# Kernel tuning notes

Hardware: AMD Instinct MI355X
Metric: run time of the kernel (lower is better)

The kernel has to match this reference:

```python
import jax, jax.numpy as jnp
import numpy as np

N_NODES = 170000
N_EDGES = 1200000
IN_DIM = 64
OUT_DIM = 40


def setup_inputs() -> dict:
    key = jax.random.key(0)
    k1, k2, k3, k4 = jax.random.split(key, 4)
    feats = jax.random.normal(k1, (N_NODES, IN_DIM), dtype=jnp.float32)
    # Linear layer params (Kaiming-ish scale)
    W = jax.random.normal(k2, (OUT_DIM, IN_DIM), dtype=jnp.float32) * (1.0 / np.sqrt(IN_DIM))
    b = jnp.zeros((OUT_DIM,), dtype=jnp.float32)
    src = jax.random.randint(k3, (N_EDGES,), 0, N_NODES, dtype=jnp.int64)
    dst = jax.random.randint(k4, (N_EDGES,), 0, N_NODES, dtype=jnp.int64)
    return {"feats": feats, "W": W, "b": b, "src": src, "dst": dst}


def reference(feats, W, b, src, dst):
    # DGL SGConv, k=1: symmetric normalization by in-degree^-1/2 on both sides.
    n = feats.shape[0]
    deg = jax.ops.segment_sum(jnp.ones_like(dst, dtype=feats.dtype), dst, num_segments=n)
    norm = jax.lax.rsqrt(jnp.maximum(deg, 1.0))  # clamp(min=1)
    h = feats * norm[:, None]                    # [N, D] pre-scale
    msgs = jnp.take(h, src, axis=0)              # [E, D] gather
    agg = jax.ops.segment_sum(msgs, dst, num_segments=n)  # [N, D] scatter-sum
    h = agg * norm[:, None]                      # post-scale
    out = jnp.einsum('nd,cd->nc', h, W) + b      # Linear(IN_DIM -> OUT_DIM)
    return out
```

## Files before the change

kernel.cpp:

```cpp
#include <hip/hip_runtime.h>
#include <hip/hip_bf16.h>

#define N_NODES 170000
#define N_EDGES 1200000
#define IN_DIM 64
#define OUT_DIM 40
#define PAD 32
#define ZW 20
#define MTILES (N_NODES / 16)
#define TFB ((MTILES + 3) / 4)
#define SEGS 8
#define SEG_SZ (N_NODES / SEGS)
#define SLICES 512
#define SLICE_E ((N_EDGES + SLICES - 1) / SLICES)
#define FILLB (SLICES * SEGS)
#define FUSED_BLOCKS (FILLB + TFB)
#define WS_DS32_OFF 36056576ULL
#define WS_SS32_OFF (WS_DS32_OFF + (size_t)N_EDGES * 4)
#define WS_NEED     (WS_SS32_OFF + (size_t)N_EDGES * 4)

typedef __attribute__((ext_vector_type(8))) short short8;
typedef __attribute__((ext_vector_type(4))) float f32x4;

__device__ __forceinline__ float bf2f(unsigned int u) {
    union { unsigned int i; float f; } v;
    v.i = u << 16;
    return v.f;
}

__device__ __forceinline__ unsigned short f2bf_bits(float x) {
    __hip_bfloat16 h = __float2bfloat16(x);
    union { __hip_bfloat16 h; unsigned short u; } c; c.h = h;
    return c.u;
}

__device__ __forceinline__ int load_idx(const void* p, int e, int is_i32) {
    return is_i32 ? ((const int*)p)[e] : (int)((const long long*)p)[e];
}

__global__ void __launch_bounds__(256) k_init(
    const unsigned short* __restrict__ Wraw, const unsigned short* __restrict__ braw,
    const unsigned int* __restrict__ dstraw, const unsigned int* __restrict__ srcraw,
    int* __restrict__ flags, unsigned short* __restrict__ Wb, float* __restrict__ bfv,
    int* __restrict__ cnt, int* __restrict__ ds32, int* __restrict__ ss32) {
    int tid = blockIdx.x * 256 + threadIdx.x;
    int gsz = (int)gridDim.x * 256;
    int4* c4 = (int4*)cnt;
    for (int i = tid; i < 42500; i += gsz) c4[i] = make_int4(0, 0, 0, 0);

    __shared__ int s_i32l;
    if (threadIdx.x == 0) s_i32l = 0;
    __syncthreads();
    if (dstraw[2 * threadIdx.x + 1] != 0u) atomicOr(&s_i32l, 1);
    __syncthreads();
    int is_i32 = s_i32l;

    if (!is_i32 && ds32) {
        const long long* d64 = (const long long*)dstraw;
        const long long* s64 = (const long long*)srcraw;
        for (int i = tid; i < N_EDGES; i += gsz) ds32[i] = (int)d64[i];
        for (int i = tid; i < N_EDGES; i += gsz) ss32[i] = (int)s64[i];
    }
    if (blockIdx.x != 0) return;

    __shared__ int s_f32;
    if (threadIdx.x == 0) s_f32 = 0;
    __syncthreads();
    for (int i = threadIdx.x; i < OUT_DIM * IN_DIM; i += 256) {
        float v = bf2f(Wraw[i]);
        if (!(fabsf(v) <= 100.0f)) atomicOr(&s_f32, 1);
    }
    __syncthreads();
    int is_f32 = s_f32;
    if (threadIdx.x == 0) { flags[0] = s_f32; flags[1] = is_i32; }
    for (int i = threadIdx.x; i < OUT_DIM * IN_DIM; i += 256)
        Wb[i] = is_f32 ? f2bf_bits(((const float*)Wraw)[i]) : Wraw[i];
    for (int i = threadIdx.x; i < OUT_DIM; i += 256)
        bfv[i] = is_f32 ? ((const float*)braw)[i] : bf2f(braw[i]);
}

__global__ void __launch_bounds__(256) k_fused(
    const void* __restrict__ src, const void* __restrict__ dst,
    int* __restrict__ cnt, int* __restrict__ slots,
    const void* __restrict__ feats, const unsigned short* __restrict__ Wb,
    unsigned short* __restrict__ Zp16, const int* __restrict__ flags,
    const int* __restrict__ ds32, const int* __restrict__ ss32) {
    int bid = blockIdx.x;
    int do_fill, id;
    if (bid < 2 * TFB) { do_fill = bid & 1; id = bid >> 1; }
    else               { do_fill = 1;       id = bid - TFB; }

    if (do_fill) {
        int is_i32 = flags[1];
        int seg   = id & 7;
        int slice = id >> 3;
        int lo = seg * SEG_SZ, hi = lo + SEG_SZ;
        int e0 = slice * SLICE_E;
        int e1 = e0 + SLICE_E; if (e1 > N_EDGES) e1 = N_EDGES;
        const int* dp = is_i32 ? (const int*)dst : ds32;
        const int* sp = is_i32 ? (const int*)src : ss32;
        if (dp) {
            int nE = e1 - e0;
            int nV = nE >> 2;
            const int4* dv = (const int4*)(dp + e0);
            const int4* sv = (const int4*)(sp + e0);
            for (int q = (int)threadIdx.x; q < nV; q += 256) {
                int4 d4 = dv[q];
                int4 s4 = sv[q];
                if (d4.x >= lo && d4.x < hi) {
                    int pos = atomicAdd(&cnt[d4.x], 1);
                    if (pos < PAD) slots[(size_t)d4.x * PAD + pos] = s4.x;
                }
                if (d4.y >= lo && d4.y < hi) {
                    int pos = atomicAdd(&cnt[d4.y], 1);
                    if (pos < PAD) slots[(size_t)d4.y * PAD + pos] = s4.y;
                }
                if (d4.z >= lo && d4.z < hi) {
                    int pos = atomicAdd(&cnt[d4.z], 1);
                    if (pos < PAD) slots[(size_t)d4.z * PAD + pos] = s4.z;
                }
                if (d4.w >= lo && d4.w < hi) {
                    int pos = atomicAdd(&cnt[d4.w], 1);
                    if (pos < PAD) slots[(size_t)d4.w * PAD + pos] = s4.w;
                }
            }
            int rem = nE & 3;
            if ((int)threadIdx.x < rem) {
                int e = e0 + (nV << 2) + (int)threadIdx.x;
                int d = dp[e];
                if (d >= lo && d < hi) {
                    int pos = atomicAdd(&cnt[d], 1);
                    if (pos < PAD) slots[(size_t)d * PAD + pos] = sp[e];
                }
            }
        } else {
            for (int e = e0 + (int)threadIdx.x; e < e1; e += 256) {
                int d = load_idx(dst, e, 0);
                if (d >= lo && d < hi) {
                    int s = load_idx(src, e, 0);
                    int pos = atomicAdd(&cnt[d], 1);
                    if (pos < PAD) slots[(size_t)d * PAD + pos] = s;
                }
            }
        }
    } else {
        int is_f32 = flags[0];
        int wave = id * 4 + (int)(threadIdx.x >> 6);
        int lane = threadIdx.x & 63;
        if (wave >= MTILES) return;
        int m = lane & 15;
        int quad = lane >> 4;
        int node0 = wave * 16;

        short8 a0, a1;
        if (is_f32) {
            const float* frow = (const float*)feats + (size_t)(node0 + m) * IN_DIM + quad * 8;
            float4 p0 = *(const float4*)(frow + 0);
            float4 p1 = *(const float4*)(frow + 4);
            float4 p2 = *(const float4*)(frow + 32);
            float4 p3 = *(const float4*)(frow + 36);
            a0[0] = (short)f2bf_bits(p0.x); a0[1] = (short)f2bf_bits(p0.y);
            a0[2] = (short)f2bf_bits(p0.z); a0[3] = (short)f2bf_bits(p0.w);
            a0[4] = (short)f2bf_bits(p1.x); a0[5] = (short)f2bf_bits(p1.y);
            a0[6] = (short)f2bf_bits(p1.z); a0[7] = (short)f2bf_bits(p1.w);
            a1[0] = (short)f2bf_bits(p2.x); a1[1] = (short)f2bf_bits(p2.y);
            a1[2] = (short)f2bf_bits(p2.z); a1[3] = (short)f2bf_bits(p2.w);
            a1[4] = (short)f2bf_bits(p3.x); a1[5] = (short)f2bf_bits(p3.y);
            a1[6] = (short)f2bf_bits(p3.z); a1[7] = (short)f2bf_bits(p3.w);
        } else {
            const unsigned short* frow = (const unsigned short*)feats + (size_t)(node0 + m) * IN_DIM + quad * 8;
            a0 = *(const short8*)(frow);
            a1 = *(const short8*)(frow + 32);
        }

        f32x4 c0 = {0.f, 0.f, 0.f, 0.f}, c1 = c0, c2 = c0;
#pragma unroll
        for (int t = 0; t < 3; t++) {
            int n = t * 16 + m;
            bool ok = (n < OUT_DIM);
            short8 b0, b1;
#pragma unroll
            for (int j = 0; j < 8; j++) { b0[j] = 0; b1[j] = 0; }
            if (ok) {
                const unsigned short* wrow = Wb + (size_t)n * IN_DIM + quad * 8;
                b0 = *(const short8*)(wrow);
                b1 = *(const short8*)(wrow + 32);
            }
            if (t == 0) {
                c0 = __builtin_amdgcn_mfma_f32_16x16x32_bf16(a0, b0, c0, 0, 0, 0);
                c0 = __builtin_amdgcn_mfma_f32_16x16x32_bf16(a1, b1, c0, 0, 0, 0);
            } else if (t == 1) {
                c1 = __builtin_amdgcn_mfma_f32_16x16x32_bf16(a0, b0, c1, 0, 0, 0);
                c1 = __builtin_amdgcn_mfma_f32_16x16x32_bf16(a1, b1, c1, 0, 0, 0);
            } else {
                c2 = __builtin_amdgcn_mfma_f32_16x16x32_bf16(a0, b0, c2, 0, 0, 0);
                c2 = __builtin_amdgcn_mfma_f32_16x16x32_bf16(a1, b1, c2, 0, 0, 0);
            }
        }

        int r0 = quad * 4;
#pragma unroll
        for (int r = 0; r < 4; r++) {
            size_t base = (size_t)(node0 + r0 + r) * OUT_DIM;
            Zp16[base + m]      = f2bf_bits(c0[r]);
            Zp16[base + 16 + m] = f2bf_bits(c1[r]);
            if (m < 8)
                Zp16[base + 32 + m] = f2bf_bits(c2[r]);
        }
    }
}

__global__ void __launch_bounds__(256) k_gather(
    const int* __restrict__ cnt, const int* __restrict__ slots,
    const unsigned int* __restrict__ Zp, const float* __restrict__ bfv,
    float* __restrict__ out) {
    int wid = (blockIdx.x * blockDim.x + threadIdx.x) >> 6;
    int lane = threadIdx.x & 63;
    if (wid >= N_NODES) return;
    int deg = cnt[wid];
    int dc = deg > PAD ? PAD : deg;
    const int* sl = slots + (size_t)wid * PAD;
    int myslot = sl[lane & 31];

    int grp = lane / 10;
    int cidx = lane - grp * 10;
    bool lact = (grp < 6);

    float a0 = 0.f, a1 = 0.f, a2 = 0.f, a3 = 0.f;
    if (dc > 0) {
        int rounds = (dc + 5) / 6;
        bool v = lact && (grp < dc);
        int s = __shfl(myslot, (v ? grp : 0) & 31);
        uint2 r = *(const uint2*)(Zp + (size_t)s * ZW + 2 * cidx);
        int cdeg = cnt[s];
        for (int rd = 1; rd < rounds; rd++) {
            int e1 = rd * 6 + grp;
            bool v1 = lact && (e1 < dc);
            int s1 = __shfl(myslot, (v1 ? e1 : 0) & 31);
            uint2 rn = *(const uint2*)(Zp + (size_t)s1 * ZW + 2 * cidx);
            int cn = cnt[s1];
            if (v) {
                float nvs = rsqrtf(cdeg > 1 ? (float)cdeg : 1.0f);
                a0 = fmaf(bf2f(r.x & 0xFFFFu), nvs, a0);
                a1 = fmaf(bf2f(r.x >> 16),     nvs, a1);
                a2 = fmaf(bf2f(r.y & 0xFFFFu), nvs, a2);
                a3 = fmaf(bf2f(r.y >> 16),     nvs, a3);
            }
            v = v1; r = rn; cdeg = cn;
        }
        if (v) {
            float nvs = rsqrtf(cdeg > 1 ? (float)cdeg : 1.0f);
            a0 = fmaf(bf2f(r.x & 0xFFFFu), nvs, a0);
            a1 = fmaf(bf2f(r.x >> 16),     nvs, a1);
            a2 = fmaf(bf2f(r.y & 0xFFFFu), nvs, a2);
            a3 = fmaf(bf2f(r.y >> 16),     nvs, a3);
        }
    }
    float b0 = a0 + __shfl(a0, (lane + 30) & 63);
    float b1 = a1 + __shfl(a1, (lane + 30) & 63);
    float b2 = a2 + __shfl(a2, (lane + 30) & 63);
    float b3 = a3 + __shfl(a3, (lane + 30) & 63);
    float t0 = b0 + __shfl(b0, (lane + 10) & 63) + __shfl(b0, (lane + 20) & 63);
    float t1 = b1 + __shfl(b1, (lane + 10) & 63) + __shfl(b1, (lane + 20) & 63);
    float t2 = b2 + __shfl(b2, (lane + 10) & 63) + __shfl(b2, (lane + 20) & 63);
    float t3 = b3 + __shfl(b3, (lane + 10) & 63) + __shfl(b3, (lane + 20) & 63);
    if (lane < 10) {
        float nv = rsqrtf(deg > 1 ? (float)deg : 1.0f);
        float4 o;
        o.x = fmaf(t0, nv, bfv[4 * lane + 0]);
        o.y = fmaf(t1, nv, bfv[4 * lane + 1]);
        o.z = fmaf(t2, nv, bfv[4 * lane + 2]);
        o.w = fmaf(t3, nv, bfv[4 * lane + 3]);
        *reinterpret_cast<float4*>(out + (size_t)wid * OUT_DIM + 4 * lane) = o;
    }
}

extern "C" void kernel_launch(void* const* d_in, const int* in_sizes, int n_in,
                              void* d_out, int out_size, void* d_ws, size_t ws_size,
                              hipStream_t stream) {
    const void* feats = d_in[0];
    const void* W     = d_in[1];
    const void* b     = d_in[2];
    const void* src   = d_in[3];
    const void* dst   = d_in[4];

    char* ws = (char*)d_ws;
    int*            flags = (int*)(ws + 0);
    float*          bfv   = (float*)(ws + 256);
    unsigned short* Wb    = (unsigned short*)(ws + 1024);
    int*            cnt   = (int*)(ws + 16384);
    int*            slots = (int*)(ws + 696448);
    unsigned short* Zp16  = (unsigned short*)(ws + 22456448);
    unsigned int*   Zp    = (unsigned int*)(ws + 22456448);
    int*            ds32  = (ws_size >= WS_NEED) ? (int*)(ws + WS_DS32_OFF) : nullptr;
    int*            ss32  = (ws_size >= WS_NEED) ? (int*)(ws + WS_SS32_OFF) : nullptr;

    k_init<<<1024, 256, 0, stream>>>((const unsigned short*)W, (const unsigned short*)b,
                                     (const unsigned int*)dst, (const unsigned int*)src,
                                     flags, Wb, bfv, cnt, ds32, ss32);
    k_fused<<<FUSED_BLOCKS, 256, 0, stream>>>(src, dst, cnt, slots, feats, Wb, Zp16, flags, ds32, ss32);
    k_gather<<<(N_NODES * 64 + 255) / 256, 256, 0, stream>>>(cnt, slots, Zp, bfv, (float*)d_out);
}
```

Before: 201.2 us.

## Process two destination nodes per wavefront in the gather kernel

The gather kernel now assigns two destination nodes to each 64-lane wave, with three lane groups of ten per node instead of six groups on one node. This halves the number of waves and makes better use of lanes when in-degree is small (average about 7), since each node now needs about three rounds instead of six lanes sitting mostly idle. Invalid lanes now load row 0 instead of an arbitrary slot. The trade-off is that the round count follows the larger of the two degrees, so the lower-degree node's lanes idle, and there is a little more index arithmetic.

```diff
diff --git a/kernel.cpp b/kernel.cpp
--- a/kernel.cpp
+++ b/kernel.cpp
@@ -15,6 +15,7 @@
 #define SLICE_E ((N_EDGES + SLICES - 1) / SLICES)
 #define FILLB (SLICES * SEGS)
 #define FUSED_BLOCKS (FILLB + TFB)
+#define GWAVES (N_NODES / 2)
 #define WS_DS32_OFF 36056576ULL
 #define WS_SS32_OFF (WS_DS32_OFF + (size_t)N_EDGES * 4)
 #define WS_NEED     (WS_SS32_OFF + (size_t)N_EDGES * 4)
@@ -216,27 +217,41 @@
     float* __restrict__ out) {
     int wid = (blockIdx.x * blockDim.x + threadIdx.x) >> 6;
     int lane = threadIdx.x & 63;
-    if (wid >= N_NODES) return;
-    int deg = cnt[wid];
-    int dc = deg > PAD ? PAD : deg;
-    const int* sl = slots + (size_t)wid * PAD;
-    int myslot = sl[lane & 31];
+    if (wid >= GWAVES) return;
+    int nA = wid * 2, nB = nA + 1;
+
+    int deg_my = cnt[nA + (lane >> 5)];
+    int deg_ot = __shfl(deg_my, lane ^ 32);
+    int degA = (lane < 32) ? deg_my : deg_ot;
+    int degB = (lane < 32) ? deg_ot : deg_my;
+    int dcA = degA > PAD ? PAD : degA;
+    int dcB = degB > PAD ? PAD : degB;
+    int dcm = dcA > dcB ? dcA : dcB;
+
+    int myslot = slots[(size_t)(nA + (lane >> 5)) * PAD + (lane & 31)];
 
     int grp = lane / 10;
+    int g3 = grp - (grp >= 3 ? 3 : 0);
     int cidx = lane - grp * 10;
     bool lact = (grp < 6);
+    int side = (grp >= 3);
+    int dcS = side ? dcB : dcA;
+    int sbase = side * 32;
 
     float a0 = 0.f, a1 = 0.f, a2 = 0.f, a3 = 0.f;
-    if (dc > 0) {
-        int rounds = (dc + 5) / 6;
-        bool v = lact && (grp < dc);
-        int s = __shfl(myslot, (v ? grp : 0) & 31);
+    if (dcm > 0) {
+        int rounds = (dcm + 2) / 3;
+        int e = g3;
+        bool v = lact && (e < dcS);
+        int s = __shfl(myslot, sbase + (v ? e : 0));
+        s = v ? s : 0;
         uint2 r = *(const uint2*)(Zp + (size_t)s * ZW + 2 * cidx);
         int cdeg = cnt[s];
         for (int rd = 1; rd < rounds; rd++) {
-            int e1 = rd * 6 + grp;
-            bool v1 = lact && (e1 < dc);
-            int s1 = __shfl(myslot, (v1 ? e1 : 0) & 31);
+            int e1 = rd * 3 + g3;
+            bool v1 = lact && (e1 < dcS);
+            int s1 = __shfl(myslot, sbase + (v1 ? e1 : 0));
+            s1 = v1 ? s1 : 0;
             uint2 rn = *(const uint2*)(Zp + (size_t)s1 * ZW + 2 * cidx);
             int cn = cnt[s1];
             if (v) {
@@ -256,22 +271,24 @@
             a3 = fmaf(bf2f(r.y >> 16),     nvs, a3);
         }
     }
-    float b0 = a0 + __shfl(a0, (lane + 30) & 63);
-    float b1 = a1 + __shfl(a1, (lane + 30) & 63);
-    float b2 = a2 + __shfl(a2, (lane + 30) & 63);
-    float b3 = a3 + __shfl(a3, (lane + 30) & 63);
-    float t0 = b0 + __shfl(b0, (lane + 10) & 63) + __shfl(b0, (lane + 20) & 63);
-    float t1 = b1 + __shfl(b1, (lane + 10) & 63) + __shfl(b1, (lane + 20) & 63);
-    float t2 = b2 + __shfl(b2, (lane + 10) & 63) + __shfl(b2, (lane + 20) & 63);
-    float t3 = b3 + __shfl(b3, (lane + 10) & 63) + __shfl(b3, (lane + 20) & 63);
-    if (lane < 10) {
-        float nv = rsqrtf(deg > 1 ? (float)deg : 1.0f);
+    float t0 = a0 + __shfl(a0, (lane + 10) & 63) + __shfl(a0, (lane + 20) & 63);
+    float t1 = a1 + __shfl(a1, (lane + 10) & 63) + __shfl(a1, (lane + 20) & 63);
+    float t2 = a2 + __shfl(a2, (lane + 10) & 63) + __shfl(a2, (lane + 20) & 63);
+    float t3 = a3 + __shfl(a3, (lane + 10) & 63) + __shfl(a3, (lane + 20) & 63);
+
+    bool wA = (lane < 10);
+    bool wB = (lane >= 30 && lane < 40);
+    if (wA || wB) {
+        int nOut = wA ? nA : nB;
+        int ci   = wA ? lane : (lane - 30);
+        int dg   = wA ? degA : degB;
+        float nv = rsqrtf(dg > 1 ? (float)dg : 1.0f);
         float4 o;
-        o.x = fmaf(t0, nv, bfv[4 * lane + 0]);
-        o.y = fmaf(t1, nv, bfv[4 * lane + 1]);
-        o.z = fmaf(t2, nv, bfv[4 * lane + 2]);
-        o.w = fmaf(t3, nv, bfv[4 * lane + 3]);
-        *reinterpret_cast<float4*>(out + (size_t)wid * OUT_DIM + 4 * lane) = o;
+        o.x = fmaf(t0, nv, bfv[4 * ci + 0]);
+        o.y = fmaf(t1, nv, bfv[4 * ci + 1]);
+        o.z = fmaf(t2, nv, bfv[4 * ci + 2]);
+        o.w = fmaf(t3, nv, bfv[4 * ci + 3]);
+        *reinterpret_cast<float4*>(out + (size_t)nOut * OUT_DIM + 4 * ci) = o;
     }
 }
 
@@ -299,5 +316,5 @@
                                      (const unsigned int*)dst, (const unsigned int*)src,
                                      flags, Wb, bfv, cnt, ds32, ss32);
     k_fused<<<FUSED_BLOCKS, 256, 0, stream>>>(src, dst, cnt, slots, feats, Wb, Zp16, flags, ds32, ss32);
-    k_gather<<<(N_NODES * 64 + 255) / 256, 256, 0, stream>>>(cnt, slots, Zp, bfv, (float*)d_out);
-}
+    k_gather<<<(GWAVES * 64 + 255) / 256, 256, 0, stream>>>(cnt, slots, Zp, bfv, (float*)d_out);
+}
```

New measurement: 196.5 us. 2.3% less time.
